# Kernel optimization log

Measured on AMD Instinct MI355X. Metric: run time of the kernel, lower is better.

## Reference

```python
import itertools
import jax, jax.numpy as jnp
import numpy as np

FS = 16000
MAX_TAU = 40
C_SOUND = 343.0
MIC_DISTANCE_FROM_WALL = 0.5
MIN_SPEAKER_HEIGHT = 1.0
MAX_SPEAKER_HEIGHT = 2.0
ROOM = (6.0, 5.0, 3.0)
DENSITY = (0.1, 0.1, 0.1)
N_MICS = 8


def _build_geometry():
    # 8-mic circular array, radius 0.4 m, centered in the room
    ang = np.arange(N_MICS) * 2.0 * np.pi / N_MICS
    receivers = np.stack([3.0 + 0.4 * np.cos(ang),
                          2.5 + 0.4 * np.sin(ang),
                          1.5 * np.ones(N_MICS)], axis=1).astype(np.float32)  # [M,3]
    combinations = np.array(list(itertools.combinations(range(N_MICS), 2)), dtype=np.int32)  # [P,2]
    # candidate grid (same nesting order as the original list comprehension)
    xs = np.arange(MIC_DISTANCE_FROM_WALL, ROOM[0] + DENSITY[0], DENSITY[0], dtype=np.float32)
    ys = np.arange(0.0, ROOM[1] + DENSITY[1], DENSITY[1], dtype=np.float32)
    zs = np.arange(MIN_SPEAKER_HEIGHT, MAX_SPEAKER_HEIGHT + DENSITY[2], DENSITY[2], dtype=np.float32)
    grid_x = np.stack(np.meshgrid(xs, ys, zs, indexing='ij'), axis=-1).reshape(-1, 3)  # [G,3]
    # true TDOA per grid point / pair -> delay index into GCC output of length 2*MAX_TAU+1
    rp = receivers[combinations]                                   # [P,2,3]
    d = np.linalg.norm(grid_x[:, None, None, :] - rp[None], axis=-1)  # [G,P,2]
    tdoa = (d[..., 0] - d[..., 1]) / C_SOUND * FS                  # samples
    tau = np.clip(MAX_TAU + np.round(tdoa), 0, 2 * MAX_TAU).astype(np.int32)  # [G,P]
    rec_centroid = receivers.mean(axis=0)                          # [3]
    return grid_x, tau, combinations, rec_centroid


def setup_inputs() -> dict:
    key = jax.random.key(0)
    signal = jax.random.normal(key, (16, N_MICS, 4096), dtype=jnp.float32)
    grid_x, tau, combinations, rec_centroid = _build_geometry()
    return {
        "signal": signal,
        "grid_x": jnp.asarray(grid_x),
        "tau": jnp.asarray(tau),
        "combinations": jnp.asarray(combinations),
        "rec_centroid": jnp.asarray(rec_centroid),
    }


def reference(signal, grid_x, tau, combinations, rec_centroid):
    B, M, N = signal.shape
    P = combinations.shape[0]
    # GCC-PHAT per mic pair
    pairs = signal[:, combinations, :]                    # [B,P,2,N]
    S = jnp.fft.rfft(pairs, axis=-1)                      # [B,P,2,F]
    X = S[..., 0, :] * jnp.conj(S[..., 1, :])             # cross-spectrum [B,P,F]
    phat = X / (jnp.abs(X) + 1e-12)
    cc = jnp.fft.irfft(phat, n=N, axis=-1)                # [B,P,N]
    # lags -MAX_TAU..MAX_TAU -> length 2*MAX_TAU+1
    cc = jnp.concatenate([cc[..., -MAX_TAU:], cc[..., :MAX_TAU + 1]], axis=-1)  # [B,P,2T+1]
    # gather per grid point / pair (avoids materializing [B,G,P,2T+1])
    gathered = cc[:, jnp.arange(P)[None, :], tau]         # [B,G,P]
    power = gathered.sum(axis=-1)                         # SRP map [B,G]
    idx = jnp.argmax(power, axis=-1)                      # [B]
    x = grid_x[idx]                                       # [B,3]
    return x - rec_centroid
```

## Files before the change

### kernel.cpp

```cpp
#include <hip/hip_runtime.h>

#define N_FFT 4096
#define NH    2048
#define NBINS 2049
#define NLAGS 81
#define MAXTAU 40
#define NSEG  8
#define SEGLEN 256
#define PI_F 3.14159265358979323846f

__global__ __launch_bounds__(1024)
void rfft_kernel(const float* __restrict__ sig,
                 float* __restrict__ S,
                 float* __restrict__ cc, int ccN) {
    int bm  = (int)blockIdx.x;
    int tid = (int)threadIdx.x;

    __shared__ float2 data[NH];
    __shared__ float2 tw[NH / 2];

    for (int i = bm * 1024 + tid; i < ccN; i += (int)gridDim.x * 1024)
        cc[i] = 0.0f;

    {
        float sv, cv;
        sincosf(-(2.0f * PI_F / (float)NH) * (float)tid, &sv, &cv);
        tw[tid] = make_float2(cv, sv);
    }

    const float2* sp = (const float2*)(sig + (size_t)bm * N_FFT);
    for (int i = tid; i < NH; i += 1024) {
        float2 v = sp[i];
        int j = (int)(__brev((unsigned)i) >> 21);
        data[j] = v;
    }
    __syncthreads();

    for (int s = 1; s <= 11; ++s) {
        int half = 1 << (s - 1);
        int g  = tid >> (s - 1);
        int j  = tid & (half - 1);
        int i0 = (g << s) + j;
        int i1 = i0 + half;
        float2 w = tw[j << (11 - s)];
        float2 u = data[i0];
        float2 v = data[i1];
        float vr = v.x * w.x - v.y * w.y;
        float vi = v.x * w.y + v.y * w.x;
        data[i0] = make_float2(u.x + vr, u.y + vi);
        data[i1] = make_float2(u.x - vr, u.y - vi);
        __syncthreads();
    }

    float* So = S + (size_t)bm * NBINS * 2;
    for (int k = tid; k < NBINS; k += 1024) {
        float2 Zk = data[k & (NH - 1)];
        float2 Zm = data[(NH - k) & (NH - 1)];
        float er = 0.5f * (Zk.x + Zm.x);
        float ei = 0.5f * (Zk.y - Zm.y);
        float dr = Zk.x - Zm.x;
        float di = Zk.y + Zm.y;
        float orr = 0.5f * di;
        float oii = -0.5f * dr;
        float sv, cv;
        sincosf(-(2.0f * PI_F / (float)N_FFT) * (float)k, &sv, &cv);
        So[k * 2]     = er + cv * orr - sv * oii;
        So[k * 2 + 1] = ei + cv * oii + sv * orr;
    }
}

#define NCH 6
#define CHLEN 43
__global__ __launch_bounds__(256)
void phat_cc_kernel(const float* __restrict__ S,
                    const int* __restrict__ comb,
                    float* __restrict__ cc, int P) {
    int id  = (int)blockIdx.x;
    int seg = id & (NSEG - 1);
    int bp  = id >> 3;
    int b   = bp / P;
    int p   = bp % P;
    int ma = comb[p * 2 + 0];
    int mb = comb[p * 2 + 1];
    const float2* Sa = (const float2*)(S + ((size_t)(b * 8 + ma)) * NBINS * 2);
    const float2* Sb = (const float2*)(S + ((size_t)(b * 8 + mb)) * NBINS * 2);

    int k0 = seg * SEGLEN;
    int k1 = (seg == NSEG - 1) ? NBINS : (k0 + SEGLEN);

    __shared__ float2 phs[SEGLEN + 1];
    __shared__ float partCr[41 * NCH];
    __shared__ float partCi[41 * NCH];

    int tid = (int)threadIdx.x;
    for (int k = k0 + tid; k < k1; k += 256) {
        float2 a = Sa[k];
        float2 c = Sb[k];
        float Xr = a.x * c.x + a.y * c.y;
        float Xi = a.y * c.x - a.x * c.y;
        float mag = sqrtf(Xr * Xr + Xi * Xi);
        float w = (k == 0 || k == 2048) ? 1.0f : 2.0f;
        float inv = w / (mag + 1e-12f);
        phs[k - k0] = make_float2(Xr * inv, Xi * inv);
    }
    __syncthreads();

    if (tid < 41 * NCH) {
        int n = tid % 41;
        int c = tid / 41;
        int kk0 = k0 + c * CHLEN;
        int kk1 = kk0 + CHLEN;
        if (kk1 > k1) kk1 = k1;

        float step = (2.0f * PI_F / (float)N_FFT) * (float)n;
        float sv, cv;
        sincosf(step, &sv, &cv);
        float wr = cv, wi = sv;
        sincosf(step * (float)kk0, &sv, &cv);
        float rr = cv, ri = sv;

        float Cr = 0.0f, Ci = 0.0f;
        for (int k = kk0; k < kk1; ++k) {
            float2 ph = phs[k - k0];
            Cr = fmaf(ph.x, rr, Cr);
            Ci = fmaf(ph.y, ri, Ci);
            float nr = rr * wr - ri * wi;
            float ni = rr * wi + ri * wr;
            rr = nr; ri = ni;
        }
        partCr[tid] = Cr;
        partCi[tid] = Ci;
    }
    __syncthreads();

    if (tid < 41) {
        float Cr = 0.0f, Ci = 0.0f;
        #pragma unroll
        for (int c = 0; c < NCH; ++c) {
            Cr += partCr[tid + 41 * c];
            Ci += partCi[tid + 41 * c];
        }
        float* outp = cc + (size_t)bp * NLAGS;
        atomicAdd(&outp[MAXTAU + tid], Cr - Ci);
        if (tid > 0) atomicAdd(&outp[MAXTAU - tid], Cr + Ci);
    }
}

__global__ __launch_bounds__(256)
void power_argmax_kernel(const float* __restrict__ cc,
                         const int* __restrict__ tau,
                         int G, int P,
                         float* __restrict__ pval,
                         int* __restrict__ pidx, int nchunks) {
    int b     = (int)blockIdx.y;
    int chunk = (int)blockIdx.x;
    int tid   = (int)threadIdx.x;

    __shared__ float ccs[28 * NLAGS];
    const float* csrc = cc + (size_t)b * P * NLAGS;
    for (int i = tid; i < 28 * NLAGS; i += 256)
        ccs[i] = csrc[i] * (1.0f / (float)N_FFT);
    __syncthreads();

    int g = chunk * 256 + tid;
    float v = -1e30f;
    int   gi = 0x7fffffff;
    if (g < G) {
        const int4* tp = (const int4*)(tau + (size_t)g * 28);
        v = 0.0f;
        #pragma unroll
        for (int q = 0; q < 7; ++q) {
            int4 tv = tp[q];
            v += ccs[(q * 4 + 0) * NLAGS + tv.x];
            v += ccs[(q * 4 + 1) * NLAGS + tv.y];
            v += ccs[(q * 4 + 2) * NLAGS + tv.z];
            v += ccs[(q * 4 + 3) * NLAGS + tv.w];
        }
        gi = g;
    }

    #pragma unroll
    for (int off = 32; off > 0; off >>= 1) {
        float v2 = __shfl_down(v, off);
        int   i2 = __shfl_down(gi, off);
        if (v2 > v || (v2 == v && i2 < gi)) { v = v2; gi = i2; }
    }
    __shared__ float wval[4];
    __shared__ int   widx[4];
    int lane = tid & 63, wv = tid >> 6;
    if (lane == 0) { wval[wv] = v; widx[wv] = gi; }
    __syncthreads();
    if (tid == 0) {
        #pragma unroll
        for (int w = 1; w < 4; ++w) {
            float v2 = wval[w]; int i2 = widx[w];
            if (v2 > v || (v2 == v && i2 < gi)) { v = v2; gi = i2; }
        }
        pval[b * nchunks + chunk] = v;
        pidx[b * nchunks + chunk] = gi;
    }
}

__global__ void finalize_kernel(const float* __restrict__ pval,
                                const int* __restrict__ pidx, int nchunks,
                                const float* __restrict__ grid_x,
                                const float* __restrict__ rec_centroid,
                                float* __restrict__ out) {
    int b = (int)blockIdx.x;
    int l = (int)threadIdx.x;
    float v = -1e30f; int gi = 0x7fffffff;
    for (int j = l; j < nchunks; j += 64) {
        float v2 = pval[b * nchunks + j];
        int   i2 = pidx[b * nchunks + j];
        if (v2 > v || (v2 == v && i2 < gi)) { v = v2; gi = i2; }
    }
    #pragma unroll
    for (int off = 32; off > 0; off >>= 1) {
        float v2 = __shfl_down(v, off);
        int   i2 = __shfl_down(gi, off);
        if (v2 > v || (v2 == v && i2 < gi)) { v = v2; gi = i2; }
    }
    if (l == 0) {
        for (int c = 0; c < 3; ++c)
            out[b * 3 + c] = grid_x[(size_t)gi * 3 + c] - rec_centroid[c];
    }
}

extern "C" void kernel_launch(void* const* d_in, const int* in_sizes, int n_in,
                              void* d_out, int out_size, void* d_ws, size_t ws_size,
                              hipStream_t stream) {
    const float* signal       = (const float*)d_in[0];
    const float* grid_x       = (const float*)d_in[1];
    const int*   tau          = (const int*)d_in[2];
    const int*   comb         = (const int*)d_in[3];
    const float* rec_centroid = (const float*)d_in[4];
    float* out = (float*)d_out;

    int G  = in_sizes[1] / 3;
    int P  = in_sizes[3] / 2;
    int BM = in_sizes[0] / N_FFT;
    int B  = BM / 8;
    int BP = B * P;

    float* S  = (float*)d_ws;
    float* cc = S + (size_t)BM * NBINS * 2;
    int nchunks = (G + 255) / 256;
    float* pval = cc + (size_t)BP * NLAGS;
    int*   pidx = (int*)(pval + (size_t)B * nchunks);

    rfft_kernel<<<BM, 1024, 0, stream>>>(signal, S, cc, BP * NLAGS);
    phat_cc_kernel<<<BP * NSEG, 256, 0, stream>>>(S, comb, cc, P);
    power_argmax_kernel<<<dim3(nchunks, B), 256, 0, stream>>>(cc, tau, G, P, pval, pidx, nchunks);
    finalize_kernel<<<B, 64, 0, stream>>>(pval, pidx, nchunks, grid_x, rec_centroid, out);
}
```

Before: 97.14 us.

## Fuse argmax finalize into power kernel via atomic key and pad FFT shared memory

Removes the separate finalize kernel launch. Each power block packs its value and index into an order-preserving 64-bit key and applies atomicMax to it. A ticket counter then lets the last block per batch write the output. Separately, the FFT shared-memory array gets one padding element every 16 entries to reduce LDS bank conflicts in the butterfly stages. This saves one kernel launch, at the cost of global atomics and a threadfence-based last-block protocol.

```diff
diff --git a/kernel.cpp b/kernel.cpp
--- a/kernel.cpp
+++ b/kernel.cpp
@@ -8,19 +8,23 @@
 #define NSEG  8
 #define SEGLEN 256
 #define PI_F 3.14159265358979323846f
+#define PAD(i) ((i) + ((i) >> 4))
 
 __global__ __launch_bounds__(1024)
 void rfft_kernel(const float* __restrict__ sig,
                  float* __restrict__ S,
-                 float* __restrict__ cc, int ccN) {
+                 float* __restrict__ cc, int ccN,
+                 unsigned long long* __restrict__ key,
+                 int* __restrict__ ticket, int B) {
     int bm  = (int)blockIdx.x;
     int tid = (int)threadIdx.x;
 
-    __shared__ float2 data[NH];
+    __shared__ float2 data[PAD(NH - 1) + 1];
     __shared__ float2 tw[NH / 2];
 
     for (int i = bm * 1024 + tid; i < ccN; i += (int)gridDim.x * 1024)
         cc[i] = 0.0f;
+    if (bm == 0 && tid < B) { key[tid] = 0ull; ticket[tid] = 0; }
 
     {
         float sv, cv;
@@ -32,7 +36,7 @@
     for (int i = tid; i < NH; i += 1024) {
         float2 v = sp[i];
         int j = (int)(__brev((unsigned)i) >> 21);
-        data[j] = v;
+        data[PAD(j)] = v;
     }
     __syncthreads();
 
@@ -43,19 +47,19 @@
         int i0 = (g << s) + j;
         int i1 = i0 + half;
         float2 w = tw[j << (11 - s)];
-        float2 u = data[i0];
-        float2 v = data[i1];
+        float2 u = data[PAD(i0)];
+        float2 v = data[PAD(i1)];
         float vr = v.x * w.x - v.y * w.y;
         float vi = v.x * w.y + v.y * w.x;
-        data[i0] = make_float2(u.x + vr, u.y + vi);
-        data[i1] = make_float2(u.x - vr, u.y - vi);
+        data[PAD(i0)] = make_float2(u.x + vr, u.y + vi);
+        data[PAD(i1)] = make_float2(u.x - vr, u.y - vi);
         __syncthreads();
     }
 
     float* So = S + (size_t)bm * NBINS * 2;
     for (int k = tid; k < NBINS; k += 1024) {
-        float2 Zk = data[k & (NH - 1)];
-        float2 Zm = data[(NH - k) & (NH - 1)];
+        float2 Zk = data[PAD(k & (NH - 1))];
+        float2 Zm = data[PAD((NH - k) & (NH - 1))];
         float er = 0.5f * (Zk.x + Zm.x);
         float ei = 0.5f * (Zk.y - Zm.y);
         float dr = Zk.x - Zm.x;
@@ -149,9 +153,12 @@
 __global__ __launch_bounds__(256)
 void power_argmax_kernel(const float* __restrict__ cc,
                          const int* __restrict__ tau,
-                         int G, int P,
-                         float* __restrict__ pval,
-                         int* __restrict__ pidx, int nchunks) {
+                         int G, int P, int nchunks,
+                         unsigned long long* __restrict__ key,
+                         int* __restrict__ ticket,
+                         const float* __restrict__ grid_x,
+                         const float* __restrict__ rec_centroid,
+                         float* __restrict__ out) {
     int b     = (int)blockIdx.y;
     int chunk = (int)blockIdx.x;
     int tid   = (int)threadIdx.x;
@@ -176,6 +183,7 @@
             v += ccs[(q * 4 + 2) * NLAGS + tv.z];
             v += ccs[(q * 4 + 3) * NLAGS + tv.w];
         }
+        v += 0.0f;
         gi = g;
     }
 
@@ -187,6 +195,7 @@
     }
     __shared__ float wval[4];
     __shared__ int   widx[4];
+    __shared__ int   lastflag;
     int lane = tid & 63, wv = tid >> 6;
     if (lane == 0) { wval[wv] = v; widx[wv] = gi; }
     __syncthreads();
@@ -196,33 +205,23 @@
             float v2 = wval[w]; int i2 = widx[w];
             if (v2 > v || (v2 == v && i2 < gi)) { v = v2; gi = i2; }
         }
-        pval[b * nchunks + chunk] = v;
-        pidx[b * nchunks + chunk] = gi;
-    }
-}
-
-__global__ void finalize_kernel(const float* __restrict__ pval,
-                                const int* __restrict__ pidx, int nchunks,
-                                const float* __restrict__ grid_x,
-                                const float* __restrict__ rec_centroid,
-                                float* __restrict__ out) {
-    int b = (int)blockIdx.x;
-    int l = (int)threadIdx.x;
-    float v = -1e30f; int gi = 0x7fffffff;
-    for (int j = l; j < nchunks; j += 64) {
-        float v2 = pval[b * nchunks + j];
-        int   i2 = pidx[b * nchunks + j];
-        if (v2 > v || (v2 == v && i2 < gi)) { v = v2; gi = i2; }
-    }
-    #pragma unroll
-    for (int off = 32; off > 0; off >>= 1) {
-        float v2 = __shfl_down(v, off);
-        int   i2 = __shfl_down(gi, off);
-        if (v2 > v || (v2 == v && i2 < gi)) { v = v2; gi = i2; }
-    }
-    if (l == 0) {
+        unsigned fb = __float_as_uint(v);
+        unsigned u  = (fb & 0x80000000u) ? ~fb : (fb | 0x80000000u);
+        unsigned long long k =
+            ((unsigned long long)u << 32) |
+            (unsigned long long)(0xffffffffu - (unsigned)gi);
+        atomicMax(&key[b], k);
+        __threadfence();
+        int old = atomicAdd(&ticket[b], 1);
+        lastflag = (old == nchunks - 1) ? 1 : 0;
+    }
+    __syncthreads();
+    if (lastflag && tid == 0) {
+        __threadfence();
+        unsigned long long k = atomicOr(&key[b], 0ull);
+        unsigned fgi = 0xffffffffu - (unsigned)(k & 0xffffffffu);
         for (int c = 0; c < 3; ++c)
-            out[b * 3 + c] = grid_x[(size_t)gi * 3 + c] - rec_centroid[c];
+            out[b * 3 + c] = grid_x[(size_t)fgi * 3 + c] - rec_centroid[c];
     }
 }
 
@@ -244,12 +243,12 @@
 
     float* S  = (float*)d_ws;
     float* cc = S + (size_t)BM * NBINS * 2;
+    unsigned long long* key = (unsigned long long*)(cc + (size_t)BP * NLAGS);
+    int* ticket = (int*)(key + B);
     int nchunks = (G + 255) / 256;
-    float* pval = cc + (size_t)BP * NLAGS;
-    int*   pidx = (int*)(pval + (size_t)B * nchunks);
-
-    rfft_kernel<<<BM, 1024, 0, stream>>>(signal, S, cc, BP * NLAGS);
+
+    rfft_kernel<<<BM, 1024, 0, stream>>>(signal, S, cc, BP * NLAGS, key, ticket, B);
     phat_cc_kernel<<<BP * NSEG, 256, 0, stream>>>(S, comb, cc, P);
-    power_argmax_kernel<<<dim3(nchunks, B), 256, 0, stream>>>(cc, tau, G, P, pval, pidx, nchunks);
-    finalize_kernel<<<B, 64, 0, stream>>>(pval, pidx, nchunks, grid_x, rec_centroid, out);
-}
+    power_argmax_kernel<<<dim3(nchunks, B), 256, 0, stream>>>(
+        cc, tau, G, P, nchunks, key, ticket, grid_x, rec_centroid, out);
+}
```

Measured after the change: 133.1 us. +37.0%, slower.
